# Optimization experiments

Measured on AMD Instinct MI355X. Metric: run time of the kernel, lower is better.

## Reference

```python
import jax, jax.numpy as jnp
import numpy as np

DEPTH, HEADS, DHEAD, DIM, MLP, RED = 4, 8, 64, 512, 2048, 128
B, P, N = 8, 4, 256


def layer_norm(x, g, b, eps=1e-5):
    m = x.mean(-1, keepdims=True)
    v = ((x - m) ** 2).mean(-1, keepdims=True)
    return (x - m) * jax.lax.rsqrt(v + eps) * g + b


def setup_inputs() -> dict:
    key = jax.random.key(0)
    ks = jax.random.split(key, 24)
    s = 0.02
    inp = {
        "x": jax.random.normal(ks[0], (B, P, N, DIM), jnp.float32),
        # per-layer stacked params (leading axis = depth)
        "ln1_g": jnp.ones((DEPTH, DIM)), "ln1_b": jnp.zeros((DEPTH, DIM)),
        "w_qkv": jax.random.normal(ks[1], (DEPTH, DIM, 3 * HEADS * DHEAD)) * s,
        "w_o": jax.random.normal(ks[2], (DEPTH, HEADS * DHEAD, DIM)) * s,
        "b_o": jnp.zeros((DEPTH, DIM)),
        "ln2_g": jnp.ones((DEPTH, DIM)), "ln2_b": jnp.zeros((DEPTH, DIM)),
        "w1": jax.random.normal(ks[3], (DEPTH, DIM, MLP)) * s, "b1": jnp.zeros((DEPTH, MLP)),
        "w2": jax.random.normal(ks[4], (DEPTH, MLP, DIM)) * s, "b2": jnp.zeros((DEPTH, DIM)),
        # BiAttn params
        "bn_g": jnp.ones((DEPTH, DIM)), "bn_b": jnp.zeros((DEPTH, DIM)),
        "wg": jax.random.normal(ks[5], (DEPTH, DIM, RED)) * s, "bg": jnp.zeros((DEPTH, RED)),
        "wl": jax.random.normal(ks[6], (DEPTH, DIM, RED)) * s, "bl": jnp.zeros((DEPTH, RED)),
        "wc": jax.random.normal(ks[7], (DEPTH, RED, DIM)) * s, "bc": jnp.zeros((DEPTH, DIM)),
        "ws": jax.random.normal(ks[8], (DEPTH, 2 * RED, 1)) * s, "bs": jnp.zeros((DEPTH, 1)),
    }
    return inp


def _attention(x, w_qkv, w_o, b_o):
    b, p, n, _ = x.shape
    qkv = jnp.einsum('bpnd,de->bpne', x, w_qkv)
    q, k, v = jnp.split(qkv, 3, axis=-1)
    def heads(t):
        return t.reshape(b, p, n, HEADS, DHEAD).transpose(0, 1, 3, 2, 4)  # b p h n d
    q, k, v = heads(q), heads(k), heads(v)
    scale = DHEAD ** -0.5
    dots = jnp.einsum('bphnd,bphmd->bphnm', q, k) * scale
    attn = jax.nn.softmax(dots, axis=-1)
    out = jnp.einsum('bphnm,bphmd->bphnd', attn, v)
    out = out.transpose(0, 1, 3, 2, 4).reshape(b, p, n, HEADS * DHEAD)
    return jnp.einsum('bpne,ed->bpnd', out, w_o) + b_o


def _biattn(x, bn_g, bn_b, wg, bg, wl, bl, wc, bc, ws, bs):
    ori = x
    x = layer_norm(x, bn_g, bn_b)
    x_global = x.mean(axis=1, keepdims=True)              # [b,1,n,dim]  (mean over p!)
    x_global = jax.nn.gelu(x_global @ wg + bg, approximate=False)  # [b,1,n,red]
    x_local = jax.nn.gelu(x @ wl + bl, approximate=False)          # [b,p,n,red]
    c_attn = jax.nn.sigmoid(x_global @ wc + bc)           # [b,1,n,dim]
    expand_g = jnp.broadcast_to(x_global, x_local.shape)
    fusion = jnp.concatenate([x_local, expand_g], axis=-1)
    s_attn = jax.nn.sigmoid(fusion @ ws + bs)             # [b,p,n,1]
    return ori * (c_attn * s_attn)


def _mlp(x, w1, b1, w2, b2, bn_g, bn_b, wg, bg, wl, bl, wc, bc, ws, bs):
    h = jax.nn.gelu(x @ w1 + b1, approximate=False)
    h = h @ w2 + b2
    return _biattn(h, bn_g, bn_b, wg, bg, wl, bl, wc, bc, ws, bs)


def reference(x, ln1_g, ln1_b, w_qkv, w_o, b_o, ln2_g, ln2_b, w1, b1, w2, b2,
              bn_g, bn_b, wg, bg, wl, bl, wc, bc, ws, bs):
    for i in range(DEPTH):
        x = _attention(layer_norm(x, ln1_g[i], ln1_b[i]), w_qkv[i], w_o[i], b_o[i]) + x
        x = _mlp(layer_norm(x, ln2_g[i], ln2_b[i]), w1[i], b1[i], w2[i], b2[i],
                 bn_g[i], bn_b[i], wg[i], bg[i], wl[i], bl[i], wc[i], bc[i], ws[i], bs[i]) + x
    return x
```

## Files before the change

### kernel.cpp

```cpp
#include <hip/hip_runtime.h>
#include <hip/hip_bf16.h>
#include <math.h>

typedef __hip_bfloat16 bf16;
typedef unsigned short u16;
typedef __bf16 bf16x8 __attribute__((ext_vector_type(8)));
typedef float f32x4 __attribute__((ext_vector_type(4)));

__device__ __forceinline__ float b2f(bf16 v) { return __bfloat162float(v); }
__device__ __forceinline__ bf16 f2b(float v) { return __float2bfloat16(v); }
__device__ __forceinline__ float bits2f(unsigned int u) {
    union { unsigned int i; float f; } w; w.i = u << 16; return w.f;
}
__device__ __forceinline__ u16 f2bits(float v) {
    union { bf16 h; u16 u; } w; w.h = __float2bfloat16(v); return w.u;
}
__device__ __forceinline__ void async16(void* lds, const void* g) {
    __builtin_amdgcn_global_load_lds(
        (const __attribute__((address_space(1))) unsigned int*)g,
        (__attribute__((address_space(3))) unsigned int*)lds, 16, 0, 0);
}

#define DEPTH 4
#define HEADS 8
#define DHEAD 64
#define DIM 512
#define MLPD 2048
#define RED 128
#define BB 8
#define PP 4
#define NN 256
#define ROWS (BB*PP*NN)
#define XELEMS ((size_t)ROWS*DIM)

__global__ __launch_bounds__(256)
void wtrans_fused(const float* __restrict__ Wqkv, u16* __restrict__ Tqkv,
                  const float* __restrict__ Wo,   u16* __restrict__ To,
                  const float* __restrict__ W1,   u16* __restrict__ T1,
                  const float* __restrict__ W2,   u16* __restrict__ T2,
                  const float* __restrict__ Wl,   u16* __restrict__ Tl,
                  const float* __restrict__ Wg,   u16* __restrict__ Tg,
                  const float* __restrict__ Wc,   u16* __restrict__ Tc)
{
    __shared__ float T[32][33];
    const int x = blockIdx.x, l = blockIdx.z;
    const float* W; u16* WT; int K, N, nx, local;
    if      (x < 768)  { W=Wqkv; WT=Tqkv; K=512;  N=1536; nx=48; local=x; }
    else if (x < 1024) { W=Wo;   WT=To;   K=512;  N=512;  nx=16; local=x-768; }
    else if (x < 2048) { W=W1;   WT=T1;   K=512;  N=2048; nx=64; local=x-1024; }
    else if (x < 3072) { W=W2;   WT=T2;   K=2048; N=512;  nx=16; local=x-2048; }
    else if (x < 3136) { W=Wl;   WT=Tl;   K=512;  N=128;  nx=4;  local=x-3072; }
    else if (x < 3200) { W=Wg;   WT=Tg;   K=512;  N=128;  nx=4;  local=x-3136; }
    else               { W=Wc;   WT=Tc;   K=128;  N=512;  nx=16; local=x-3200; }
    W  += (size_t)l * K * N;
    WT += (size_t)l * N * K;
    const int n0 = (local % nx) * 32, k0 = (local / nx) * 32;
    const int tx = threadIdx.x & 31, ty = threadIdx.x >> 5;
#pragma unroll
    for (int r = 0; r < 4; ++r)
        T[ty + r*8][tx] = W[(size_t)(k0 + ty + r*8) * N + n0 + tx];
    __syncthreads();
#pragma unroll
    for (int r = 0; r < 4; ++r)
        WT[(size_t)(n0 + ty + r*8) * K + k0 + tx] = f2bits(T[tx][ty + r*8]);
}

template<int BM, int BN, int BK, int WROWS, int WCOLS>
__global__ __launch_bounds__(256)
void gemm_db(const u16* __restrict__ A, const u16* __restrict__ WT,
             const float* __restrict__ bias, const float* __restrict__ res,
             void* __restrict__ Cv, int M, int N, int K, int act, int outf32)
{
    constexpr int KG  = BK/8;
    constexpr int RPC = 512/BK;
    constexpr int NCA = BM*BK/512;
    constexpr int NCB = BN*BK/512;
    constexpr int CPT = (NCA+NCB)/4;
    constexpr int WM = BM/WROWS, WN = BN/WCOLS;
    constexpr int AM = WM/16, AN = WN/16, KB = BK/32;

    __shared__ u16 As[2][BM*BK];
    __shared__ u16 Bs[2][BN*BK];
    const int tid = threadIdx.x, wave = tid >> 6, lane = tid & 63;
    const int bm = blockIdx.x * BM;
    const int bn = blockIdx.y * BN;
    const int wm = (wave / WCOLS) * WM, wn = (wave % WCOLS) * WN;
    const int lr = lane & 15, quad = lane >> 4;

    const int rowc = lane / KG;
    const int kgs  = ((lane & (KG-1)) ^ (KG == 4 ? ((rowc >> 1) & 3) : (rowc & 7))) * 8;

    auto stage = [&](int buf, int k0) {
#pragma unroll
        for (int t = 0; t < CPT; ++t) {
            const int c = wave*CPT + t;
            if (c < NCA)
                async16(&As[buf][c*512], A  + (size_t)(bm + c*RPC + rowc) * K + k0 + kgs);
            else
                async16(&Bs[buf][(c-NCA)*512], WT + (size_t)(bn + (c-NCA)*RPC + rowc) * K + k0 + kgs);
        }
    };

    f32x4 acc[AM][AN] = {};

    stage(0, 0);
    __syncthreads();

    const int NK = K / BK;
    for (int ki = 0; ki < NK; ++ki) {
        const int cur = ki & 1;
        if (ki + 1 < NK) stage(cur ^ 1, (ki + 1) * BK);

        bf16x8 af[AM][KB], bv[AN][KB];
#pragma unroll
        for (int i = 0; i < AM; ++i) {
            const int rA = wm + i*16 + lr;
            const int sw = (KG == 4 ? (((rA & 15) >> 1) & 3) : (rA & 7));
#pragma unroll
            for (int kb = 0; kb < KB; ++kb)
                af[i][kb] = *(const bf16x8*)(As[cur] + rA*BK + (((kb*4 + quad) ^ sw) * 8));
        }
#pragma unroll
        for (int j = 0; j < AN; ++j) {
            const int rB = wn + j*16 + lr;
            const int sw = (KG == 4 ? (((rB & 15) >> 1) & 3) : (rB & 7));
#pragma unroll
            for (int kb = 0; kb < KB; ++kb)
                bv[j][kb] = *(const bf16x8*)(Bs[cur] + rB*BK + (((kb*4 + quad) ^ sw) * 8));
        }
#pragma unroll
        for (int i = 0; i < AM; ++i)
#pragma unroll
            for (int j = 0; j < AN; ++j)
#pragma unroll
                for (int kb = 0; kb < KB; ++kb)
                    acc[i][j] = __builtin_amdgcn_mfma_f32_16x16x32_bf16(
                        af[i][kb], bv[j][kb], acc[i][j], 0, 0, 0);
        __syncthreads();
    }

#pragma unroll
    for (int i = 0; i < AM; ++i) {
        const int rowb = bm + wm + i*16 + quad*4;
#pragma unroll
        for (int j = 0; j < AN; ++j) {
            const int col = bn + wn + j*16 + lr;
            const float bvs = bias ? bias[col] : 0.f;
#pragma unroll
            for (int r = 0; r < 4; ++r) {
                float v = acc[i][j][r] + bvs;
                if (act == 1) v = 0.5f * v * (1.0f + erff(v * 0.70710678118f));
                else if (act == 2) v = 1.0f / (1.0f + __expf(-v));
                const size_t idx = (size_t)(rowb + r) * N + col;
                if (res) v += res[idx];
                if (outf32) ((float*)Cv)[idx] = v;
                else        ((u16*)Cv)[idx] = f2bits(v);
            }
        }
    }
}

__global__ __launch_bounds__(256)
void gemm_wlg(const u16* __restrict__ L, const u16* __restrict__ G,
              const u16* __restrict__ WTl, const u16* __restrict__ WTg,
              const float* __restrict__ bl, const float* __restrict__ bg,
              u16* __restrict__ XL, u16* __restrict__ G2)
{
    constexpr int K = 512, N = 128;
    const u16* A; const u16* WT; const float* bias; u16* C;
    int bm, bn;
    const int blk = blockIdx.x;
    if (blk < 256) { A = L; WT = WTl; bias = bl; C = XL;
                     bm = (blk & 127) * 64; bn = (blk >> 7) * 64; }
    else           { const int b2 = blk - 256; A = G; WT = WTg; bias = bg; C = G2;
                     bm = (b2 & 31) * 64; bn = (b2 >> 5) * 64; }

    __shared__ u16 As[2][64*64];
    __shared__ u16 Bs[2][64*64];
    const int tid = threadIdx.x, wave = tid >> 6, lane = tid & 63;
    const int wm = (wave >> 1) * 32, wn = (wave & 1) * 32;
    const int lr = lane & 15, quad = lane >> 4;

    const int rowc = lane >> 3;
    const int kgs  = ((lane & 7) ^ (rowc & 7)) * 8;

    auto stage = [&](int buf, int k0) {
#pragma unroll
        for (int t = 0; t < 4; ++t) {
            const int c = wave*4 + t;
            if (c < 8) async16(&As[buf][c*512], A  + (size_t)(bm + c*8 + rowc) * K + k0 + kgs);
            else       async16(&Bs[buf][(c-8)*512], WT + (size_t)(bn + (c-8)*8 + rowc) * K + k0 + kgs);
        }
    };

    f32x4 acc[2][2] = {};
    stage(0, 0);
    __syncthreads();

    for (int ki = 0; ki < 8; ++ki) {
        const int cur = ki & 1;
        if (ki + 1 < 8) stage(cur ^ 1, (ki + 1) * 64);

        bf16x8 af[2][2], bv[2][2];
#pragma unroll
        for (int i = 0; i < 2; ++i) {
            const int rA = wm + i*16 + lr;
            const int sw = rA & 7;
#pragma unroll
            for (int kb = 0; kb < 2; ++kb)
                af[i][kb] = *(const bf16x8*)(As[cur] + rA*64 + (((kb*4 + quad) ^ sw) * 8));
        }
#pragma unroll
        for (int j = 0; j < 2; ++j) {
            const int rB = wn + j*16 + lr;
            const int sw = rB & 7;
#pragma unroll
            for (int kb = 0; kb < 2; ++kb)
                bv[j][kb] = *(const bf16x8*)(Bs[cur] + rB*64 + (((kb*4 + quad) ^ sw) * 8));
        }
#pragma unroll
        for (int i = 0; i < 2; ++i)
#pragma unroll
            for (int j = 0; j < 2; ++j)
#pragma unroll
                for (int kb = 0; kb < 2; ++kb)
                    acc[i][j] = __builtin_amdgcn_mfma_f32_16x16x32_bf16(
                        af[i][kb], bv[j][kb], acc[i][j], 0, 0, 0);
        __syncthreads();
    }

#pragma unroll
    for (int i = 0; i < 2; ++i) {
        const int rowb = bm + wm + i*16 + quad*4;
#pragma unroll
        for (int j = 0; j < 2; ++j) {
            const int col = bn + wn + j*16 + lr;
            const float bvs = bias[col];
#pragma unroll
            for (int r = 0; r < 4; ++r) {
                float v = acc[i][j][r] + bvs;
                v = 0.5f * v * (1.0f + erff(v * 0.70710678118f));
                C[(size_t)(rowb + r) * N + col] = f2bits(v);
            }
        }
    }
}

__global__ __launch_bounds__(256)
void attn_mfma(const u16* __restrict__ qkv, u16* __restrict__ out)
{
    __shared__ u16 Kt[64*72];
    __shared__ u16 Vt[64*72];
    __shared__ u16 Pw[4][16*72];
    const int tid = threadIdx.x;
    const int wave = tid >> 6, lane = tid & 63;
    const int lr = lane & 15, quad = lane >> 4;
    const int bp = blockIdx.x >> 5;
    const int h  = (blockIdx.x >> 2) & 7;
    const int qq = blockIdx.x & 3;
    const u16* base = qkv + (size_t)bp * NN * (3*DIM);
    const int qo = h*DHEAD, ko = DIM + h*DHEAD, vo = 2*DIM + h*DHEAD;
    const int m0 = qq*64 + wave*16;

    bf16x8 qf[2];
#pragma unroll
    for (int kb = 0; kb < 2; ++kb)
        qf[kb] = *(const bf16x8*)(base + (size_t)(m0 + lr)*(3*DIM) + qo + kb*32 + quad*8);

    f32x4 o[4] = {};
    float mrow[4], lrow[4];
#pragma unroll
    for (int r = 0; r < 4; ++r) { mrow[r] = -1e30f; lrow[r] = 0.f; }

    const int sr = tid >> 3, sc = tid & 7;

    for (int t = 0; t < 4; ++t) {
        __syncthreads();
#pragma unroll
        for (int half = 0; half < 2; ++half) {
            const int key = half*32 + sr;
            const u16* krow = base + (size_t)(t*64 + key)*(3*DIM);
            uint4 kv = *(const uint4*)(krow + ko + sc*8);
            *(uint4*)(Kt + key*72 + sc*8) = kv;
            uint4 vv = *(const uint4*)(krow + vo + sc*8);
            const int d0 = sc*8;
            Vt[(d0+0)*72 + key] = (u16)(vv.x & 0xffffu);
            Vt[(d0+1)*72 + key] = (u16)(vv.x >> 16);
            Vt[(d0+2)*72 + key] = (u16)(vv.y & 0xffffu);
            Vt[(d0+3)*72 + key] = (u16)(vv.y >> 16);
            Vt[(d0+4)*72 + key] = (u16)(vv.z & 0xffffu);
            Vt[(d0+5)*72 + key] = (u16)(vv.z >> 16);
            Vt[(d0+6)*72 + key] = (u16)(vv.w & 0xffffu);
            Vt[(d0+7)*72 + key] = (u16)(vv.w >> 16);
        }
        __syncthreads();

        f32x4 s[4] = {};
        bf16x8 kf[4][2];
#pragma unroll
        for (int j = 0; j < 4; ++j)
#pragma unroll
            for (int kb = 0; kb < 2; ++kb)
                kf[j][kb] = *(const bf16x8*)(Kt + (j*16 + lr)*72 + kb*32 + quad*8);
#pragma unroll
        for (int j = 0; j < 4; ++j)
#pragma unroll
            for (int kb = 0; kb < 2; ++kb)
                s[j] = __builtin_amdgcn_mfma_f32_16x16x32_bf16(
                    qf[kb], kf[j][kb], s[j], 0, 0, 0);

        float alpha[4];
#pragma unroll
        for (int r = 0; r < 4; ++r) {
#pragma unroll
            for (int j = 0; j < 4; ++j) s[j][r] *= 0.125f;
            float mt = fmaxf(fmaxf(s[0][r], s[1][r]), fmaxf(s[2][r], s[3][r]));
#pragma unroll
            for (int off = 1; off <= 8; off <<= 1) mt = fmaxf(mt, __shfl_xor(mt, off));
            const float mn = fmaxf(mrow[r], mt);
            alpha[r] = __expf(mrow[r] - mn);
            mrow[r] = mn;
            float ssum = 0.f;
#pragma unroll
            for (int j = 0; j < 4; ++j) {
                const float p = __expf(s[j][r] - mn);
                s[j][r] = p; ssum += p;
            }
#pragma unroll
            for (int off = 1; off <= 8; off <<= 1) ssum += __shfl_xor(ssum, off);
            lrow[r] = lrow[r]*alpha[r] + ssum;
        }

#pragma unroll
        for (int j = 0; j < 4; ++j)
#pragma unroll
            for (int r = 0; r < 4; ++r)
                Pw[wave][(quad*4 + r)*72 + j*16 + lr] = f2bits(s[j][r]);
        __syncthreads();

#pragma unroll
        for (int jd = 0; jd < 4; ++jd)
#pragma unroll
            for (int r = 0; r < 4; ++r)
                o[jd][r] *= alpha[r];

        bf16x8 af[2], bv[4][2];
#pragma unroll
        for (int kb = 0; kb < 2; ++kb)
            af[kb] = *(const bf16x8*)(Pw[wave] + lr*72 + kb*32 + quad*8);
#pragma unroll
        for (int jd = 0; jd < 4; ++jd)
#pragma unroll
            for (int kb = 0; kb < 2; ++kb)
                bv[jd][kb] = *(const bf16x8*)(Vt + (jd*16 + lr)*72 + kb*32 + quad*8);
#pragma unroll
        for (int jd = 0; jd < 4; ++jd)
#pragma unroll
            for (int kb = 0; kb < 2; ++kb)
                o[jd] = __builtin_amdgcn_mfma_f32_16x16x32_bf16(
                    af[kb], bv[jd][kb], o[jd], 0, 0, 0);
    }

#pragma unroll
    for (int r = 0; r < 4; ++r) {
        const float inv = 1.0f / lrow[r];
        const size_t rowg = (size_t)bp*NN + m0 + quad*4 + r;
#pragma unroll
        for (int jd = 0; jd < 4; ++jd)
            out[rowg*DIM + h*DHEAD + jd*16 + lr] = f2bits(o[jd][r] * inv);
    }
}

__global__ __launch_bounds__(256)
void ln_kernel(const float* __restrict__ x, const float* __restrict__ g,
               const float* __restrict__ b, u16* __restrict__ y, int rows)
{
    const int wave = threadIdx.x >> 6, lane = threadIdx.x & 63;
    const int row = blockIdx.x * 4 + wave;
    if (row >= rows) return;
    const float4* xr = (const float4*)(x + (size_t)row * DIM);
    float4 v0 = xr[lane], v1 = xr[lane + 64];
    float s  = v0.x+v0.y+v0.z+v0.w + v1.x+v1.y+v1.z+v1.w;
    float s2 = v0.x*v0.x+v0.y*v0.y+v0.z*v0.z+v0.w*v0.w
             + v1.x*v1.x+v1.y*v1.y+v1.z*v1.z+v1.w*v1.w;
#pragma unroll
    for (int off = 32; off; off >>= 1) { s += __shfl_xor(s, off); s2 += __shfl_xor(s2, off); }
    const float mean = s * (1.f/512.f);
    const float var  = s2 * (1.f/512.f) - mean*mean;
    const float rstd = rsqrtf(var + 1e-5f);
    const float4* gp = (const float4*)g; const float4* bp = (const float4*)b;
    float4 g0 = gp[lane], g1 = gp[lane+64], b0 = bp[lane], b1 = bp[lane+64];
    ushort4 o0, o1;
    o0.x = f2bits((v0.x-mean)*rstd*g0.x + b0.x);
    o0.y = f2bits((v0.y-mean)*rstd*g0.y + b0.y);
    o0.z = f2bits((v0.z-mean)*rstd*g0.z + b0.z);
    o0.w = f2bits((v0.w-mean)*rstd*g0.w + b0.w);
    o1.x = f2bits((v1.x-mean)*rstd*g1.x + b1.x);
    o1.y = f2bits((v1.y-mean)*rstd*g1.y + b1.y);
    o1.z = f2bits((v1.z-mean)*rstd*g1.z + b1.z);
    o1.w = f2bits((v1.w-mean)*rstd*g1.w + b1.w);
    ushort4* yr = (ushort4*)(y + (size_t)row * DIM);
    yr[lane] = o0; yr[lane+64] = o1;
}

__global__ __launch_bounds__(256)
void lnmean_kernel(const float* __restrict__ x, const float* __restrict__ g,
                   const float* __restrict__ b, u16* __restrict__ y,
                   u16* __restrict__ G)
{
    __shared__ float T[4][512];
    const int wave = threadIdx.x >> 6, lane = threadIdx.x & 63;
    const int bb = blockIdx.x >> 8, n = blockIdx.x & 255;
    const int row = (bb*PP + wave)*NN + n;
    const float4* xr = (const float4*)(x + (size_t)row * DIM);
    float4 v0 = xr[lane], v1 = xr[lane + 64];
    float s  = v0.x+v0.y+v0.z+v0.w + v1.x+v1.y+v1.z+v1.w;
    float s2 = v0.x*v0.x+v0.y*v0.y+v0.z*v0.z+v0.w*v0.w
             + v1.x*v1.x+v1.y*v1.y+v1.z*v1.z+v1.w*v1.w;
#pragma unroll
    for (int off = 32; off; off >>= 1) { s += __shfl_xor(s, off); s2 += __shfl_xor(s2, off); }
    const float mean = s * (1.f/512.f);
    const float var  = s2 * (1.f/512.f) - mean*mean;
    const float rstd = rsqrtf(var + 1e-5f);
    const float4* gp = (const float4*)g; const float4* bp = (const float4*)b;
    float4 g0 = gp[lane], g1 = gp[lane+64], b0 = bp[lane], b1 = bp[lane+64];
    float4 y0, y1;
    y0.x = (v0.x-mean)*rstd*g0.x + b0.x;
    y0.y = (v0.y-mean)*rstd*g0.y + b0.y;
    y0.z = (v0.z-mean)*rstd*g0.z + b0.z;
    y0.w = (v0.w-mean)*rstd*g0.w + b0.w;
    y1.x = (v1.x-mean)*rstd*g1.x + b1.x;
    y1.y = (v1.y-mean)*rstd*g1.y + b1.y;
    y1.z = (v1.z-mean)*rstd*g1.z + b1.z;
    y1.w = (v1.w-mean)*rstd*g1.w + b1.w;
    ushort4 o0, o1;
    o0.x = f2bits(y0.x); o0.y = f2bits(y0.y); o0.z = f2bits(y0.z); o0.w = f2bits(y0.w);
    o1.x = f2bits(y1.x); o1.y = f2bits(y1.y); o1.z = f2bits(y1.z); o1.w = f2bits(y1.w);
    ushort4* yr = (ushort4*)(y + (size_t)row * DIM);
    yr[lane] = o0; yr[lane+64] = o1;
    *(float4*)&T[wave][lane*4]       = y0;
    *(float4*)&T[wave][256 + lane*4] = y1;
    __syncthreads();
    const int d0 = threadIdx.x;
    const float m0 = (T[0][d0]     + T[1][d0]     + T[2][d0]     + T[3][d0])     * 0.25f;
    const float m1 = (T[0][d0+256] + T[1][d0+256] + T[2][d0+256] + T[3][d0+256]) * 0.25f;
    u16* gr = G + ((size_t)bb*NN + n)*DIM;
    gr[d0]       = f2bits(m0);
    gr[d0 + 256] = f2bits(m1);
}

__global__ __launch_bounds__(256)
void fuse2_kernel(const float4* __restrict__ xb, const float4* __restrict__ m1,
                  const u16* __restrict__ ca, const u16* __restrict__ xl,
                  const u16* __restrict__ xg, const float* __restrict__ wsv,
                  const float* __restrict__ bs, float4* __restrict__ xa,
                  const float* __restrict__ lng, const float* __restrict__ lnb,
                  u16* __restrict__ lnout)
{
    const int wave = threadIdx.x >> 6, lane = threadIdx.x & 63;
    const int row = blockIdx.x * 4 + wave;
    const int b = row >> 10, n = row & 255;
    const u16* xlr = xl + (size_t)row * RED;
    const u16* xgr = xg + ((size_t)b*NN + n) * RED;
    float s = bits2f(xlr[lane])    * wsv[lane]
            + bits2f(xlr[lane+64]) * wsv[lane+64]
            + bits2f(xgr[lane])    * wsv[RED+lane]
            + bits2f(xgr[lane+64]) * wsv[RED+64+lane];
#pragma unroll
    for (int off = 32; off; off >>= 1) s += __shfl_xor(s, off);
    s = 1.f / (1.f + __expf(-(s + bs[0])));
    const u16* car = ca + ((((size_t)b << 8) + n)*DIM);

    float4 o0, o1;
    {
        const size_t idx = (size_t)row*128 + lane;
        ushort4 cu = *(const ushort4*)(car + lane*4);
        float4 xv = xb[idx], mv = m1[idx];
        o0.x = xv.x + mv.x * bits2f(cu.x) * s;
        o0.y = xv.y + mv.y * bits2f(cu.y) * s;
        o0.z = xv.z + mv.z * bits2f(cu.z) * s;
        o0.w = xv.w + mv.w * bits2f(cu.w) * s;
        xa[idx] = o0;
    }
    {
        const size_t idx = (size_t)row*128 + lane + 64;
        ushort4 cu = *(const ushort4*)(car + (lane + 64)*4);
        float4 xv = xb[idx], mv = m1[idx];
        o1.x = xv.x + mv.x * bits2f(cu.x) * s;
        o1.y = xv.y + mv.y * bits2f(cu.y) * s;
        o1.z = xv.z + mv.z * bits2f(cu.z) * s;
        o1.w = xv.w + mv.w * bits2f(cu.w) * s;
        xa[idx] = o1;
    }

    if (lnout) {
        float t  = o0.x+o0.y+o0.z+o0.w + o1.x+o1.y+o1.z+o1.w;
        float t2 = o0.x*o0.x+o0.y*o0.y+o0.z*o0.z+o0.w*o0.w
                 + o1.x*o1.x+o1.y*o1.y+o1.z*o1.z+o1.w*o1.w;
#pragma unroll
        for (int off = 32; off; off >>= 1) { t += __shfl_xor(t, off); t2 += __shfl_xor(t2, off); }
        const float mean = t * (1.f/512.f);
        const float var  = t2 * (1.f/512.f) - mean*mean;
        const float rstd = rsqrtf(var + 1e-5f);
        const float4* gp = (const float4*)lng; const float4* bp = (const float4*)lnb;
        float4 g0 = gp[lane], g1 = gp[lane+64], b0 = bp[lane], b1 = bp[lane+64];
        ushort4 q0, q1;
        q0.x = f2bits((o0.x-mean)*rstd*g0.x + b0.x);
        q0.y = f2bits((o0.y-mean)*rstd*g0.y + b0.y);
        q0.z = f2bits((o0.z-mean)*rstd*g0.z + b0.z);
        q0.w = f2bits((o0.w-mean)*rstd*g0.w + b0.w);
        q1.x = f2bits((o1.x-mean)*rstd*g1.x + b1.x);
        q1.y = f2bits((o1.y-mean)*rstd*g1.y + b1.y);
        q1.z = f2bits((o1.z-mean)*rstd*g1.z + b1.z);
        q1.w = f2bits((o1.w-mean)*rstd*g1.w + b1.w);
        ushort4* yr = (ushort4*)(lnout + (size_t)row * DIM);
        yr[lane] = q0; yr[lane+64] = q1;
    }
}

extern "C" void kernel_launch(void* const* d_in, const int* in_sizes, int n_in,
                              void* d_out, int out_size, void* d_ws, size_t ws_size,
                              hipStream_t stream)
{
    const float* x_in  = (const float*)d_in[0];
    const float* ln1_g = (const float*)d_in[1];
    const float* ln1_b = (const float*)d_in[2];
    const float* w_qkv = (const float*)d_in[3];
    const float* w_o   = (const float*)d_in[4];
    const float* b_o   = (const float*)d_in[5];
    const float* ln2_g = (const float*)d_in[6];
    const float* ln2_b = (const float*)d_in[7];
    const float* w1    = (const float*)d_in[8];
    const float* b1    = (const float*)d_in[9];
    const float* w2    = (const float*)d_in[10];
    const float* b2    = (const float*)d_in[11];
    const float* bn_g  = (const float*)d_in[12];
    const float* bn_b  = (const float*)d_in[13];
    const float* wg    = (const float*)d_in[14];
    const float* bg    = (const float*)d_in[15];
    const float* wl    = (const float*)d_in[16];
    const float* bl    = (const float*)d_in[17];
    const float* wc    = (const float*)d_in[18];
    const float* bc    = (const float*)d_in[19];
    const float* wsw   = (const float*)d_in[20];
    const float* bsb   = (const float*)d_in[21];

    char* ws = (char*)d_ws;
    auto alloc = [&](size_t bytes) {
        char* p = ws;
        ws += (bytes + 255) & ~(size_t)255;
        return p;
    };
    float* XA = (float*)alloc(XELEMS * 4);
    float* XB = (float*)alloc(XELEMS * 4);
    float* M1 = (float*)alloc(XELEMS * 4);
    u16*   L  = (u16*)  alloc(XELEMS * 2);
    u16*   Q  = (u16*)  alloc((size_t)ROWS * 3*DIM * 2);
    u16*   H  = (u16*)  alloc((size_t)ROWS * MLPD * 2);
    u16*   G  = (u16*)  alloc((size_t)BB*NN*DIM * 2);
    u16*   G2 = (u16*)  alloc((size_t)BB*NN*RED * 2);
    u16*   XL = (u16*)  alloc((size_t)ROWS*RED * 2);
    u16*   CA = (u16*)  alloc((size_t)BB*NN*DIM * 2);
    u16* WTqkv = (u16*)alloc((size_t)DEPTH*DIM*3*DIM * 2);
    u16* WTo   = (u16*)alloc((size_t)DEPTH*DIM*DIM * 2);
    u16* WT1   = (u16*)alloc((size_t)DEPTH*DIM*MLPD * 2);
    u16* WT2   = (u16*)alloc((size_t)DEPTH*MLPD*DIM * 2);
    u16* WTl   = (u16*)alloc((size_t)DEPTH*DIM*RED * 2);
    u16* WTg   = (u16*)alloc((size_t)DEPTH*DIM*RED * 2);
    u16* WTc   = (u16*)alloc((size_t)DEPTH*RED*DIM * 2);

    wtrans_fused<<<dim3(3264, 1, DEPTH), 256, 0, stream>>>(
        w_qkv, WTqkv, w_o, WTo, w1, WT1, w2, WT2, wl, WTl, wg, WTg, wc, WTc);

    ln_kernel<<<ROWS/4, 256, 0, stream>>>(x_in, ln1_g, ln1_b, L, ROWS);

    for (int l = 0; l < DEPTH; ++l) {
        const float* Xres = l ? (const float*)XA : x_in;
        gemm_db<64,64,64,2,2><<<dim3(128,24), 256, 0, stream>>>(
            L, WTqkv + (size_t)l*DIM*3*DIM, nullptr, nullptr, Q, ROWS, 3*DIM, DIM, 0, 0);
        attn_mfma<<<BB*PP*HEADS*4, 256, 0, stream>>>(Q, L);
        gemm_db<64,64,64,2,2><<<dim3(128,8), 256, 0, stream>>>(
            L, WTo + (size_t)l*DIM*DIM, b_o + l*DIM, Xres, XB, ROWS, DIM, DIM, 0, 1);

        ln_kernel<<<ROWS/4, 256, 0, stream>>>(XB, ln2_g + l*DIM, ln2_b + l*DIM, Q, ROWS);
        gemm_db<64,64,32,2,2><<<dim3(128,32), 256, 0, stream>>>(
            Q, WT1 + (size_t)l*DIM*MLPD, b1 + l*MLPD, nullptr, H, ROWS, MLPD, DIM, 1, 0);
        gemm_db<64,64,64,2,2><<<dim3(128,8), 256, 0, stream>>>(
            H, WT2 + (size_t)l*MLPD*DIM, b2 + l*DIM, nullptr, M1, ROWS, DIM, MLPD, 0, 1);

        lnmean_kernel<<<BB*NN, 256, 0, stream>>>(M1, bn_g + l*DIM, bn_b + l*DIM, L, G);
        gemm_wlg<<<320, 256, 0, stream>>>(L, G, WTl + (size_t)l*DIM*RED,
                                          WTg + (size_t)l*DIM*RED,
                                          bl + l*RED, bg + l*RED, XL, G2);
        gemm_db<64,64,64,2,2><<<dim3(32,8), 256, 0, stream>>>(
            G2, WTc + (size_t)l*RED*DIM, bc + l*DIM, nullptr, CA, BB*NN, DIM, RED, 2, 0);
        const int last = (l == DEPTH-1);
        fuse2_kernel<<<ROWS/4, 256, 0, stream>>>(
            (const float4*)XB, (const float4*)M1, CA, XL, G2,
            wsw + (size_t)l*2*RED, bsb + l,
            last ? (float4*)d_out : (float4*)XA,
            ln1_g + (l+1)*DIM, ln1_b + (l+1)*DIM,
            last ? nullptr : L);
    }
}
```

Before: 836.3 us.

## Add 256x256-tile 8-wave GEMM for the MLP up-projection

Adds a new gemm_8ph kernel with 256x256 block tiles, 512 threads and 8 waves. Four waves load A and four load B through async global-to-LDS copies, double-buffered. The MFMA work is split into four phases separated by barriers, with raised wave priority, and it is used for the first MLP GEMM (8192x2048x512) in place of the 64x64 gemm_db. Larger tiles give more reuse per LDS load, but the launch is only 256 blocks, which may underfill the GPU, and the 128 KB of LDS per block limits occupancy.

Measured after the change: 862.3 us. +3.1%, slower.

```diff
diff --git a/kernel.cpp b/kernel.cpp
--- a/kernel.cpp
+++ b/kernel.cpp
@@ -144,6 +144,112 @@
         const int rowb = bm + wm + i*16 + quad*4;
 #pragma unroll
         for (int j = 0; j < AN; ++j) {
+            const int col = bn + wn + j*16 + lr;
+            const float bvs = bias ? bias[col] : 0.f;
+#pragma unroll
+            for (int r = 0; r < 4; ++r) {
+                float v = acc[i][j][r] + bvs;
+                if (act == 1) v = 0.5f * v * (1.0f + erff(v * 0.70710678118f));
+                else if (act == 2) v = 1.0f / (1.0f + __expf(-v));
+                const size_t idx = (size_t)(rowb + r) * N + col;
+                if (res) v += res[idx];
+                if (outf32) ((float*)Cv)[idx] = v;
+                else        ((u16*)Cv)[idx] = f2bits(v);
+            }
+        }
+    }
+}
+
+__global__ __launch_bounds__(512, 1)
+void gemm_8ph(const u16* __restrict__ A, const u16* __restrict__ WT,
+              const float* __restrict__ bias, const float* __restrict__ res,
+              void* __restrict__ Cv, int M, int N, int K, int act, int outf32)
+{
+    __shared__ u16 As[2][256*64];
+    __shared__ u16 Bs[2][256*64];
+    const int tid = threadIdx.x, wave = tid >> 6, lane = tid & 63;
+    const int bm = blockIdx.x * 256;
+    const int bn = blockIdx.y * 256;
+    const int wm = (wave >> 2) * 128;
+    const int wn = (wave & 3) * 64;
+    const int lr = lane & 15, quad = lane >> 4;
+
+    const int rowc = lane >> 3;
+    const int kgs  = ((lane & 7) ^ (rowc & 7)) * 8;
+
+    auto stage = [&](int buf, int k0) {
+        if (wave < 4) {
+#pragma unroll
+            for (int t = 0; t < 8; ++t) {
+                const int c = wave*8 + t;
+                async16(&As[buf][c*512], A + (size_t)(bm + c*8 + rowc) * K + k0 + kgs);
+            }
+        } else {
+#pragma unroll
+            for (int t = 0; t < 8; ++t) {
+                const int c = (wave - 4)*8 + t;
+                async16(&Bs[buf][c*512], WT + (size_t)(bn + c*8 + rowc) * K + k0 + kgs);
+            }
+        }
+    };
+
+    f32x4 acc[8][4] = {};
+
+    stage(0, 0);
+    const int NK = K / 64;
+    for (int t = 0; t < NK; ++t) {
+        const int cur = t & 1;
+        if (t + 1 < NK) {
+            stage(cur ^ 1, (t + 1) * 64);
+            asm volatile("s_waitcnt vmcnt(8)" ::: "memory");
+        } else {
+            asm volatile("s_waitcnt vmcnt(0)" ::: "memory");
+        }
+        __builtin_amdgcn_s_barrier();
+
+        bf16x8 bv[4][2];
+#pragma unroll
+        for (int j = 0; j < 4; ++j) {
+            const int rB = wn + j*16 + lr;
+            const int sw = rB & 7;
+#pragma unroll
+            for (int kb = 0; kb < 2; ++kb)
+                bv[j][kb] = *(const bf16x8*)(Bs[cur] + rB*64 + (((kb*4 + quad) ^ sw) * 8));
+        }
+
+#pragma unroll
+        for (int p = 0; p < 4; ++p) {
+            bf16x8 af[2][2];
+#pragma unroll
+            for (int ii = 0; ii < 2; ++ii) {
+                const int rA = wm + (p*2 + ii)*16 + lr;
+                const int sw = rA & 7;
+#pragma unroll
+                for (int kb = 0; kb < 2; ++kb)
+                    af[ii][kb] = *(const bf16x8*)(As[cur] + rA*64 + (((kb*4 + quad) ^ sw) * 8));
+            }
+            __builtin_amdgcn_s_barrier();
+            asm volatile("s_waitcnt lgkmcnt(0)" ::: "memory");
+            __builtin_amdgcn_sched_barrier(0);
+            __builtin_amdgcn_s_setprio(1);
+#pragma unroll
+            for (int ii = 0; ii < 2; ++ii)
+#pragma unroll
+                for (int j = 0; j < 4; ++j)
+#pragma unroll
+                    for (int kb = 0; kb < 2; ++kb)
+                        acc[p*2 + ii][j] = __builtin_amdgcn_mfma_f32_16x16x32_bf16(
+                            af[ii][kb], bv[j][kb], acc[p*2 + ii][j], 0, 0, 0);
+            __builtin_amdgcn_s_setprio(0);
+            __builtin_amdgcn_s_barrier();
+        }
+    }
+
+#pragma unroll
+    for (int i = 0; i < 8; ++i) {
+        const int rowb = bm + wm + i*16 + quad*4;
+#pragma unroll
+        for (int j = 0; j < 4; ++j) {
             const int col = bn + wn + j*16 + lr;
             const float bvs = bias ? bias[col] : 0.f;
 #pragma unroll
@@ -583,7 +689,7 @@
             L, WTo + (size_t)l*DIM*DIM, b_o + l*DIM, Xres, XB, ROWS, DIM, DIM, 0, 1);
 
         ln_kernel<<<ROWS/4, 256, 0, stream>>>(XB, ln2_g + l*DIM, ln2_b + l*DIM, Q, ROWS);
-        gemm_db<64,64,32,2,2><<<dim3(128,32), 256, 0, stream>>>(
+        gemm_8ph<<<dim3(32,8), 512, 0, stream>>>(
             Q, WT1 + (size_t)l*DIM*MLPD, b1 + l*MLPD, nullptr, H, ROWS, MLPD, DIM, 1, 0);
         gemm_db<64,64,64,2,2><<<dim3(128,8), 256, 0, stream>>>(
             H, WT2 + (size_t)l*MLPD*DIM, b2 + l*DIM, nullptr, M1, ROWS, DIM, MLPD, 0, 1);
```
